# Kernel optimization log

Hardware: AMD Instinct MI355X
Metric: run time of the kernel (lower is better)

Reference implementation:

```python
import jax, jax.numpy as jnp
import numpy as np

# ---- module hyperparameters (from init_kwargs) ----
FREQ_RANGE = (100.0, 8000.0)
CHANNELS = 128
BW_FACTOR = 1.0
SAMPLE_RATE = 16000
ORDER = 4                    # gammatone order (4 cascaded one-pole sections)
ATT_HALF_BW_DB = -3.0        # pyfilterbank default attenuation at half bandwidth


def _hertz_to_erbscale(f):
    return 21.4 * np.log10(4.37e-3 * f + 1.0)


def _erbscale_to_hertz(e):
    return (10.0 ** (e / 21.4) - 1.0) / 4.37e-3


def _design_bank():
    """Replicates pyfilterbank.gammatone: frequencies_gammatone_bank + design_filter.
    normfreq=0 so the ERB offset term is zero."""
    sb = _hertz_to_erbscale(FREQ_RANGE[0])
    eb = _hertz_to_erbscale(FREQ_RANGE[1])
    density = (eb - sb) / (CHANNELS - 0.05)
    cf = _erbscale_to_hertz(np.arange(sb, eb, density))        # [C] center freqs (Hz)
    erb_aud = 24.7 * (4.37e-3 * cf + 1.0)                      # audiological ERB
    phi = np.pi * BW_FACTOR * erb_aud / SAMPLE_RATE
    alpha = 10.0 ** (0.1 * ATT_HALF_BW_DB / ORDER)
    p = (-2.0 + 2.0 * alpha * np.cos(phi)) / (1.0 - alpha)
    lam = -p / 2.0 - np.sqrt(p * p / 4.0 - 1.0)
    beta = 2.0 * np.pi * cf / SAMPLE_RATE
    coef = lam * np.exp(1j * beta)                             # complex pole [C]
    factor = 2.0 * (1.0 - np.abs(coef)) ** ORDER               # stage-1 gain [C]
    return coef, factor


def setup_inputs() -> dict:
    key = jax.random.key(0)
    inp = jax.random.normal(key, (8, 32000), dtype=jnp.float32)  # [B, T] waveforms
    coef, factor = _design_bank()
    return {
        "inp": inp,
        "coef_re": jnp.asarray(np.real(coef), dtype=jnp.float32),  # [C]
        "coef_im": jnp.asarray(np.imag(coef), dtype=jnp.float32),  # [C]
        "factor": jnp.asarray(factor, dtype=jnp.float32),          # [C]
    }


def reference(inp, coef_re, coef_im, factor):
    """Gammatone filterbank analysis: 4 cascaded complex one-pole IIR sections
    per band, applied to every (batch, band) pair in parallel; returns the real
    part, shaped [B, T, C] like the original module's np stacking/transpose."""
    coef = (coef_re + 1j * coef_im).astype(jnp.complex64)          # [C]
    B, T = inp.shape
    C = coef.shape[0]
    # time-major stage input: [T, B, C]; stage 1 applies the gain `factor`
    y = inp.T[:, :, None].astype(jnp.complex64) * factor.astype(jnp.complex64)
    s0 = jnp.zeros((B, C), dtype=jnp.complex64)

    def one_pole(x):
        # s[t] = coef * s[t-1] + x[t], zero initial state (lfilter zi=0)
        def step(s, xt):
            s = coef * s + xt
            return s, s
        _, out = jax.lax.scan(step, s0, x)
        return out

    for _ in range(ORDER):   # fixed small cascade, stages 2..4 have b0 = 1
        y = one_pole(y)
    return jnp.real(y).transpose(1, 0, 2).astype(jnp.float32)      # [B, T, C]
```

## Files before the change

### kernel.cpp

```cpp
#include <hip/hip_runtime.h>


typedef float f32x2 __attribute__((ext_vector_type(2)));

#define B_N    8
#define T_LEN  32000
#define C_CH   128
#define L_CHK  256
#define NB     125
#define W_MAX  1024

#define PSTEP(XR) do {                               \
    const f32x2 xin = {(XR), 0.f};                   \
    const f32x2 t4 = crr * s4 + s3;                  \
    const f32x2 t3 = crr * s3 + s2;                  \
    const f32x2 t2 = crr * s2 + s1;                  \
    const f32x2 t1 = crr * s1 + xin;                 \
    s4 = cni * s4.yx + t4;                           \
    s3 = cni * s3.yx + t3;                           \
    s2 = cni * s2.yx + t2;                           \
    s1 = cni * s1.yx + t1;                           \
} while (0)

__global__ __launch_bounds__(64) void gt_trunc(
    const float* __restrict__ x, const float* __restrict__ cre,
    const float* __restrict__ cim, const float* __restrict__ fac,
    float* __restrict__ out)
{
    __shared__ __align__(16) float xs[L_CHK + W_MAX + 8];
    const int g  = blockIdx.x;
    const int k  = blockIdx.y;
    const int b  = blockIdx.z;
    const int c  = g * 64 + threadIdx.x;
    const int t0 = k * L_CHK;

    const float cr0 = cre[g * 64], ci0 = cim[g * 64];
    const float negln = -0.5f * __logf(cr0 * cr0 + ci0 * ci0);
    int W = (int)ceilf(18.0f / negln) + 2;
    W = (W + 3) & ~3;
    if (W > W_MAX) W = W_MAX;
    int start = t0 - W;
    if (start < 0) start = 0;
    const int n  = t0 + L_CHK - start;
    const int nw = t0 - start;

    const float* xb = x + (size_t)b * T_LEN + start;
    for (int i = threadIdx.x; i < n; i += 64) xs[i + 1] = xb[i];
    if (threadIdx.x < 7) xs[n + 1 + threadIdx.x] = 0.f;

    const float cr = cre[c], ci = cim[c], f = fac[c];
    const f32x2 crr = {cr, cr};
    const f32x2 cni = {-ci, ci};
    __syncthreads();

    const f32x2 a0 = {xs[1], 0.f}, a1 = {xs[2], 0.f}, a2 = {xs[3], 0.f};
    f32x2 t, y11, s1, s2, s3, s4;
    t  = crr * a0  + a1;  y11 = cni * a0.yx  + t;
    t  = crr * y11 + a2;  s1  = cni * y11.yx + t;
    t  = crr * a0  + y11; s2  = cni * a0.yx  + t;
    s3 = a0;
    s4 = (f32x2){0.f, 0.f};

    float4 cur = *(const float4*)&xs[4];
    for (int i = 0; i < nw; i += 4) {
        const float4 nxt = *(const float4*)&xs[i + 8];
        PSTEP(cur.x); PSTEP(cur.y); PSTEP(cur.z); PSTEP(cur.w);
        cur = nxt;
    }

    float* op = out + ((size_t)b * T_LEN + t0) * C_CH + c;
    for (int i = nw; i < nw + L_CHK; i += 4) {
        const float4 nxt = *(const float4*)&xs[i + 8];
        PSTEP(cur.x); op[0 * C_CH] = s4.x * f;
        PSTEP(cur.y); op[1 * C_CH] = s4.x * f;
        PSTEP(cur.z); op[2 * C_CH] = s4.x * f;
        PSTEP(cur.w); op[3 * C_CH] = s4.x * f;
        op += 4 * (size_t)C_CH;
        cur = nxt;
    }
}

extern "C" void kernel_launch(void* const* d_in, const int* in_sizes, int n_in,
                              void* d_out, int out_size, void* d_ws, size_t ws_size,
                              hipStream_t stream) {
    const float* x   = (const float*)d_in[0];
    const float* cre = (const float*)d_in[1];
    const float* cim = (const float*)d_in[2];
    const float* fac = (const float*)d_in[3];
    float* out = (float*)d_out;

    gt_trunc<<<dim3(2, NB, B_N), 64, 0, stream>>>(x, cre, cim, fac, out);
}
```

Before: 165.9 us.

## Replace truncated warm-up windows with exact three-phase chunked scan

Replaces the per-chunk warm-up recurrence over a truncated history window with an exact parallel scan. Phase 1 computes each chunk's end state from zero initial state, a small chain kernel propagates carried states across chunks using the pole raised to the chunk length (with binomial coefficients for the 4-stage cascade), and phase 3 reruns each chunk from its true incoming state and writes outputs. This removes warm-up work of up to a thousand samples per chunk and makes the result exact. The cost is two extra launches, a serial 125-step chain kernel, and recomputing each chunk twice.

```diff
diff --git a/kernel.cpp b/kernel.cpp
--- a/kernel.cpp
+++ b/kernel.cpp
@@ -3,12 +3,11 @@
 
 typedef float f32x2 __attribute__((ext_vector_type(2)));
 
-#define B_N    8
-#define T_LEN  32000
-#define C_CH   128
-#define L_CHK  256
-#define NB     125
-#define W_MAX  1024
+#define B_N   8
+#define T_LEN 32000
+#define C_CH  128
+#define L_CHK 256
+#define NKC   125
 
 #define PSTEP(XR) do {                               \
     const f32x2 xin = {(XR), 0.f};                   \
@@ -22,61 +21,125 @@
     s1 = cni * s1.yx + t1;                           \
 } while (0)
 
-__global__ __launch_bounds__(64) void gt_trunc(
+#define CMADD(DST, S, ADD) do {                      \
+    const f32x2 _t = crr * (S) + (ADD);              \
+    DST = cni * (S).yx + _t;                         \
+} while (0)
+
+__device__ inline f32x2 cmul(f32x2 a, f32x2 s) {
+    return (f32x2){a.x * s.x - a.y * s.y, a.x * s.y + a.y * s.x};
+}
+
+template<int PHASE>
+__global__ __launch_bounds__(64) void gt_phase(
     const float* __restrict__ x, const float* __restrict__ cre,
     const float* __restrict__ cim, const float* __restrict__ fac,
-    float* __restrict__ out)
+    float* __restrict__ out, float* __restrict__ ws)
 {
-    __shared__ __align__(16) float xs[L_CHK + W_MAX + 8];
+    __shared__ __align__(16) float xs[L_CHK + 16];
     const int g  = blockIdx.x;
     const int k  = blockIdx.y;
     const int b  = blockIdx.z;
     const int c  = g * 64 + threadIdx.x;
     const int t0 = k * L_CHK;
+    const int n_avail = (T_LEN - t0 < L_CHK + 3) ? (T_LEN - t0) : (L_CHK + 3);
 
-    const float cr0 = cre[g * 64], ci0 = cim[g * 64];
-    const float negln = -0.5f * __logf(cr0 * cr0 + ci0 * ci0);
-    int W = (int)ceilf(18.0f / negln) + 2;
-    W = (W + 3) & ~3;
-    if (W > W_MAX) W = W_MAX;
-    int start = t0 - W;
-    if (start < 0) start = 0;
-    const int n  = t0 + L_CHK - start;
-    const int nw = t0 - start;
+    const float* xb = x + (size_t)b * T_LEN + t0;
+    for (int i = threadIdx.x; i < n_avail; i += 64) xs[i + 1] = xb[i];
+    if (threadIdx.x < 8) xs[n_avail + 1 + threadIdx.x] = 0.f;
 
-    const float* xb = x + (size_t)b * T_LEN + start;
-    for (int i = threadIdx.x; i < n; i += 64) xs[i + 1] = xb[i];
-    if (threadIdx.x < 7) xs[n + 1 + threadIdx.x] = 0.f;
-
-    const float cr = cre[c], ci = cim[c], f = fac[c];
+    const float cr = cre[c], ci = cim[c];
     const f32x2 crr = {cr, cr};
     const f32x2 cni = {-ci, ci};
+
+    f32x2 sg1 = {0.f,0.f}, sg2 = {0.f,0.f}, sg3 = {0.f,0.f}, sg4 = {0.f,0.f};
+    float* wp = ws + (((size_t)k * 8 + b) * 128 + c) * 8;
+    if constexpr (PHASE == 3) {
+        const float4 A  = *(const float4*)wp;
+        const float4 Bv = *(const float4*)(wp + 4);
+        sg1 = (f32x2){A.x,  A.y};  sg2 = (f32x2){A.z,  A.w};
+        sg3 = (f32x2){Bv.x, Bv.y}; sg4 = (f32x2){Bv.z, Bv.w};
+    }
     __syncthreads();
 
-    const f32x2 a0 = {xs[1], 0.f}, a1 = {xs[2], 0.f}, a2 = {xs[3], 0.f};
-    f32x2 t, y11, s1, s2, s3, s4;
-    t  = crr * a0  + a1;  y11 = cni * a0.yx  + t;
-    t  = crr * y11 + a2;  s1  = cni * y11.yx + t;
-    t  = crr * a0  + y11; s2  = cni * a0.yx  + t;
-    s3 = a0;
-    s4 = (f32x2){0.f, 0.f};
+    const f32x2 x0v = {xs[1], 0.f}, x1v = {xs[2], 0.f}, x2v = {xs[3], 0.f};
+    f32x2 y10, y11, y20, s1, s2, s3, s4;
+    CMADD(y10, sg1, x0v);
+    CMADD(y11, y10, x1v);
+    CMADD(s1,  y11, x2v);
+    CMADD(y20, sg2, y10);
+    CMADD(s2,  y20, y11);
+    CMADD(s3,  sg3, y20);
+    s4 = sg4;
 
     float4 cur = *(const float4*)&xs[4];
-    for (int i = 0; i < nw; i += 4) {
-        const float4 nxt = *(const float4*)&xs[i + 8];
-        PSTEP(cur.x); PSTEP(cur.y); PSTEP(cur.z); PSTEP(cur.w);
-        cur = nxt;
+    if constexpr (PHASE == 1) {
+        for (int i = 0; i < L_CHK - 4; i += 4) {
+            const float4 nxt = *(const float4*)&xs[i + 8];
+            PSTEP(cur.x); PSTEP(cur.y); PSTEP(cur.z); PSTEP(cur.w);
+            cur = nxt;
+        }
+        f32x2 sv1, sv2, sv3, sv4;
+        PSTEP(cur.x); sv1 = s1;
+        PSTEP(cur.y); sv2 = s2;
+        PSTEP(cur.z); sv3 = s3;
+        PSTEP(cur.w); sv4 = s4;
+        *(float4*)wp       = (float4){sv1.x, sv1.y, sv2.x, sv2.y};
+        *(float4*)(wp + 4) = (float4){sv3.x, sv3.y, sv4.x, sv4.y};
+    } else {
+        const float f = fac[c];
+        float* op = out + ((size_t)b * T_LEN + t0) * C_CH + c;
+        for (int i = 0; i < L_CHK; i += 4) {
+            const float4 nxt = *(const float4*)&xs[i + 8];
+            PSTEP(cur.x); op[0 * C_CH] = s4.x * f;
+            PSTEP(cur.y); op[1 * C_CH] = s4.x * f;
+            PSTEP(cur.z); op[2 * C_CH] = s4.x * f;
+            PSTEP(cur.w); op[3 * C_CH] = s4.x * f;
+            op += 4 * (size_t)C_CH;
+            cur = nxt;
+        }
     }
+}
 
-    float* op = out + ((size_t)b * T_LEN + t0) * C_CH + c;
-    for (int i = nw; i < nw + L_CHK; i += 4) {
-        const float4 nxt = *(const float4*)&xs[i + 8];
-        PSTEP(cur.x); op[0 * C_CH] = s4.x * f;
-        PSTEP(cur.y); op[1 * C_CH] = s4.x * f;
-        PSTEP(cur.z); op[2 * C_CH] = s4.x * f;
-        PSTEP(cur.w); op[3 * C_CH] = s4.x * f;
-        op += 4 * (size_t)C_CH;
-        cur = nxt;
+__global__ __launch_bounds__(64) void gt_chain(
+    const float* __restrict__ cre, const float* __restrict__ cim,
+    float* __restrict__ ws)
+{
+    const int b = blockIdx.x >> 1;
+    const int c = (blockIdx.x & 1) * 64 + threadIdx.x;
+    const float cr = cre[c], ci = cim[c];
+    float pr = cr, pi = ci;
+    #pragma unroll
+    for (int q = 0; q < 8; ++q) {
+        const float nr = pr * pr - pi * pi, ni = 2.f * pr * pi;
+        pr = nr; pi = ni;
+    }
+    const f32x2 m0 = {pr, pi};
+    const f32x2 m1 = {pr * 256.f,     pi * 256.f};
+    const f32x2 m2 = {pr * 32896.f,   pi * 32896.f};
+    const f32x2 m3 = {pr * 2829056.f, pi * 2829056.f};
+
+    float* p = ws + ((size_t)b * 128 + c) * 8;
+    const size_t KS = (size_t)8 * 128 * 8;
+    float4 A0 = *(const float4*)p,          B0 = *(const float4*)(p + 4);
+    float4 A1 = *(const float4*)(p + KS),   B1 = *(const float4*)(p + KS + 4);
+    f32x2 s1 = {0,0}, s2 = {0,0}, s3 = {0,0}, s4 = {0,0};
+    for (int k = 0; k < NKC; ++k) {
+        const f32x2 d1 = {A0.x, A0.y}, d2 = {A0.z, A0.w};
+        const f32x2 d3 = {B0.x, B0.y}, d4 = {B0.z, B0.w};
+        *(float4*)p       = (float4){s1.x, s1.y, s2.x, s2.y};
+        *(float4*)(p + 4) = (float4){s3.x, s3.y, s4.x, s4.y};
+        A0 = A1; B0 = B1;
+        if (k < NKC - 2) {
+            A1 = *(const float4*)(p + 2 * KS);
+            B1 = *(const float4*)(p + 2 * KS + 4);
+        }
+        const f32x2 n4 = cmul(m0,s4) + cmul(m1,s3) + cmul(m2,s2) + cmul(m3,s1) + d4;
+        const f32x2 n3 = cmul(m0,s3) + cmul(m1,s2) + cmul(m2,s1) + d3;
+        const f32x2 n2 = cmul(m0,s2) + cmul(m1,s1) + d2;
+        const f32x2 n1 = cmul(m0,s1) + d1;
+        s1 = n1; s2 = n2; s3 = n3; s4 = n4;
+        p += KS;
     }
 }
 
@@ -88,6 +151,9 @@
     const float* cim = (const float*)d_in[2];
     const float* fac = (const float*)d_in[3];
     float* out = (float*)d_out;
+    float* ws  = (float*)d_ws;
 
-    gt_trunc<<<dim3(2, NB, B_N), 64, 0, stream>>>(x, cre, cim, fac, out);
+    gt_phase<1><<<dim3(2, NKC, B_N), 64, 0, stream>>>(x, cre, cim, fac, out, ws);
+    gt_chain   <<<16, 64, 0, stream>>>(cre, cim, ws);
+    gt_phase<3><<<dim3(2, NKC, B_N), 64, 0, stream>>>(x, cre, cim, fac, out, ws);
 }
```

Result: slower. 196.3 us (+18.3%).
